# Kernel tuning notes

Measured on AMD Instinct MI355X. Metric: run time of the kernel, lower is better.

Reference implementation:

```python
import jax, jax.numpy as jnp
import numpy as np

N_NODES = 50000
N_EDGES = 800000
IN_DIM = 128
HID = 128
NUM_GRAPHS = 64


def setup_inputs() -> dict:
    key = jax.random.key(0)
    ks = jax.random.split(key, 10)
    x = jax.random.normal(ks[0], (N_NODES, IN_DIM), dtype=jnp.float32)
    edge_index = jax.random.randint(ks[1], (2, N_EDGES), 0, N_NODES, dtype=jnp.int64)
    batch = jnp.sort(jax.random.randint(ks[2], (N_NODES,), 0, NUM_GRAPHS, dtype=jnp.int64))
    s = 1.0 / np.sqrt(IN_DIM)
    W0 = jax.random.uniform(ks[3], (IN_DIM, HID), jnp.float32, -s, s)
    b0 = jnp.zeros((HID,), jnp.float32)
    s = 1.0 / np.sqrt(HID)
    W1 = jax.random.uniform(ks[4], (HID, HID), jnp.float32, -s, s)
    b1 = jnp.zeros((HID,), jnp.float32)
    W2 = jax.random.uniform(ks[5], (HID, HID), jnp.float32, -s, s)
    b2 = jnp.zeros((HID,), jnp.float32)
    return {"x": x, "edge_index": edge_index, "batch": batch,
            "W0": W0, "b0": b0, "W1": W1, "b1": b1, "W2": W2, "b2": b2}


def reference(x, edge_index, batch, W0, b0, W1, b1, W2, b2):
    N = x.shape[0]
    # GCNConv: add self loops, symmetric degree normalization
    loop = jnp.arange(N, dtype=edge_index.dtype)
    src = jnp.concatenate([edge_index[0], loop])  # [E+N]
    dst = jnp.concatenate([edge_index[1], loop])
    deg = jax.ops.segment_sum(jnp.ones_like(dst, dtype=x.dtype), dst, num_segments=N)
    dinv = jnp.where(deg > 0, jax.lax.rsqrt(deg), 0.0)
    norm = (dinv[src] * dinv[dst])[:, None]  # [E+N, 1]

    def gcn_layer(h, W, b):
        h = h @ W  # [N, hid]
        agg = jax.ops.segment_sum(h[src] * norm, dst, num_segments=N)
        return agg + b

    h = jax.nn.relu(gcn_layer(x, W0, b0))
    h = jax.nn.relu(gcn_layer(h, W1, b1))
    h = jax.nn.relu(gcn_layer(h, W2, b2))
    # dropout is identity at inference (training=False)

    # global_mean_pool by batch index
    sums = jax.ops.segment_sum(h, batch, num_segments=NUM_GRAPHS)
    counts = jax.ops.segment_sum(jnp.ones((N,), h.dtype), batch, num_segments=NUM_GRAPHS)
    return sums / jnp.maximum(counts, 1.0)[:, None]
```

## Files before the change

kernel.cpp:

```cpp
#include <hip/hip_runtime.h>
#include <hip/hip_bf16.h>

#define NNODES 50000
#define NEDGES 800000
#define HIDDIM 128
#define NGRAPH 64
#define BUCKET 64

typedef __attribute__((ext_vector_type(8))) short short8;
typedef __attribute__((ext_vector_type(4))) float floatx4;
typedef __attribute__((ext_vector_type(4))) unsigned short ushortx4;
typedef __attribute__((ext_vector_type(4))) unsigned int uintx4;

__device__ __forceinline__ float bfbits2f(unsigned short u) {
    return __uint_as_float(((unsigned int)u) << 16);
}
__device__ __forceinline__ unsigned short f2bfbits(float v) {
    __hip_bfloat16 h = __float2bfloat16(v);
    return __builtin_bit_cast(unsigned short, h);
}
__device__ __forceinline__ float bflo(unsigned int w) { return __uint_as_float(w << 16); }
__device__ __forceinline__ float bfhi(unsigned int w) { return __uint_as_float(w & 0xffff0000u); }

__global__ void k_detect(const unsigned int* __restrict__ xw,
                         const unsigned int* __restrict__ eiw,
                         int* __restrict__ flags) {
    __shared__ int sh_hit, sh_zero;
    int t = threadIdx.x;
    if (t == 0) { sh_hit = 0; sh_zero = 0; }
    __syncthreads();
    if (t < 128) {
        unsigned int w = xw[t * 97 + 5];
        int e = (int)((w >> 7) & 0xFF);
        if (e >= 110 && e <= 140) atomicAdd(&sh_hit, 1);
        if (eiw[1001 + 2 * t] == 0) atomicAdd(&sh_zero, 1);
    }
    __syncthreads();
    if (t == 0) {
        flags[0] = (sh_hit >= 64) ? 1 : 0;
        flags[1] = (sh_zero >= 120) ? 1 : 0;
    }
}

__global__ void k_init(const unsigned int* __restrict__ xw,
                       const unsigned int* __restrict__ eiw,
                       int* __restrict__ flags, int* __restrict__ cnt) {
    __shared__ int sh_hit, sh_zero;
    int t = threadIdx.x;
    int i = blockIdx.x * 256 + t;
    if (i < 50176) cnt[i] = 0;
    if (blockIdx.x != 0) return;
    if (t == 0) { sh_hit = 0; sh_zero = 0; }
    __syncthreads();
    if (t < 128) {
        unsigned int w = xw[t * 97 + 5];
        int e = (int)((w >> 7) & 0xFF);
        if (e >= 110 && e <= 140) atomicAdd(&sh_hit, 1);
        if (eiw[1001 + 2 * t] == 0) atomicAdd(&sh_zero, 1);
    }
    __syncthreads();
    if (t == 0) {
        flags[0] = (sh_hit >= 64) ? 1 : 0;
        flags[1] = (sh_zero >= 120) ? 1 : 0;
    }
}

__device__ __forceinline__ int ld_idx(const int* __restrict__ p, int j, int wide) {
    return wide ? p[2 * j] : p[j];
}

__global__ __launch_bounds__(256) void k_append(const int* __restrict__ ei,
                                                const int* __restrict__ bat,
                                                const int* __restrict__ flags,
                                                int* __restrict__ cnt,
                                                unsigned short* __restrict__ ecol,
                                                int* __restrict__ bounds) {
    if (blockIdx.x == gridDim.x - 1) {
        int g = threadIdx.x;
        if (g > NGRAPH) return;
        int wide = flags[1];
        int lo = 0, hi = NNODES;
        while (lo < hi) {
            int mid = (lo + hi) >> 1;
            if (ld_idx(bat, mid, wide) < g) lo = mid + 1; else hi = mid;
        }
        bounds[g] = lo;
        return;
    }
    int T = blockIdx.x * 256 + threadIdx.x;
    int e0 = T * 8;
    if (e0 >= NEDGES) return;
    int wide = flags[1];
    int s[8], d[8];
    if (wide) {
        const int4* __restrict__ sp = (const int4*)ei;
        const int4* __restrict__ dp = (const int4*)(ei + 2 * NEDGES);
#pragma unroll
        for (int q = 0; q < 4; ++q) {
            int4 sv = sp[T * 4 + q]; s[2 * q] = sv.x; s[2 * q + 1] = sv.z;
            int4 dv = dp[T * 4 + q]; d[2 * q] = dv.x; d[2 * q + 1] = dv.z;
        }
    } else {
        const int4* __restrict__ sp = (const int4*)ei;
        const int4* __restrict__ dp = (const int4*)(ei + NEDGES);
#pragma unroll
        for (int q = 0; q < 2; ++q) {
            int4 sv = sp[T * 2 + q];
            s[4 * q] = sv.x; s[4 * q + 1] = sv.y; s[4 * q + 2] = sv.z; s[4 * q + 3] = sv.w;
            int4 dv = dp[T * 2 + q];
            d[4 * q] = dv.x; d[4 * q + 1] = dv.y; d[4 * q + 2] = dv.z; d[4 * q + 3] = dv.w;
        }
    }
    int p[8];
#pragma unroll
    for (int q = 0; q < 8; ++q) p[q] = atomicAdd(&cnt[d[q]], 1);
#pragma unroll
    for (int q = 0; q < 8; ++q) {
        if (p[q] < BUCKET) {
            __builtin_nontemporal_store((unsigned short)s[q],
                                        &ecol[(size_t)d[q] * BUCKET + p[q]]);
        }
    }
}

__global__ __launch_bounds__(256) void k_gemm_mfma(const void* __restrict__ A,
                                                   const void* __restrict__ W,
                                                   const int* __restrict__ flags,
                                                   int a_mode,
                                                   const int* __restrict__ degcnt,
                                                   unsigned short* __restrict__ out,
                                                   int M) {
    __shared__ __align__(16) unsigned short Wl[16 * 128 * 8];
    __shared__ __align__(16) unsigned short Alds[64 * 17 * 8];
    const int tid = threadIdx.x;
    const int F = flags[0];
    const int abf = (a_mode == 2) ? 1 : (a_mode == 1 ? F : 0);
    const int row0 = blockIdx.x * 64;

    if (F) {
        const ushort4* __restrict__ Wg = (const ushort4*)W;
#pragma unroll
        for (int it = 0; it < 16; ++it) {
            int idx = it * 256 + tid;
            int k = idx >> 5, n = (idx & 31) * 4;
            ushort4 wv = Wg[idx];
            unsigned short* dst = &Wl[(((k >> 3) * 128) + n) * 8 + (k & 7)];
            dst[0] = wv.x; dst[8] = wv.y; dst[16] = wv.z; dst[24] = wv.w;
        }
    } else {
        const float4* __restrict__ Wg = (const float4*)W;
#pragma unroll
        for (int it = 0; it < 16; ++it) {
            int idx = it * 256 + tid;
            int k = idx >> 5, n = (idx & 31) * 4;
            float4 wv = Wg[idx];
            unsigned short* dst = &Wl[(((k >> 3) * 128) + n) * 8 + (k & 7)];
            dst[0] = f2bfbits(wv.x); dst[8]  = f2bfbits(wv.y);
            dst[16] = f2bfbits(wv.z); dst[24] = f2bfbits(wv.w);
        }
    }
    if (abf) {
#pragma unroll
        for (int it = 0; it < 4; ++it) {
            int idx = it * 256 + tid;
            int m = idx >> 4, kb = idx & 15;
            int gr = row0 + m;
            uint4 v = make_uint4(0, 0, 0, 0);
            if (gr < M) v = ((const uint4*)A)[(size_t)gr * 16 + kb];
            *reinterpret_cast<uint4*>(&Alds[(m * 17 + kb) * 8]) = v;
        }
    } else {
#pragma unroll
        for (int it = 0; it < 8; ++it) {
            int idx = it * 256 + tid;
            int m = idx >> 5, k4 = idx & 31;
            int k = k4 * 4;
            int gr = row0 + m;
            float4 v = make_float4(0, 0, 0, 0);
            if (gr < M) v = ((const float4*)A)[(size_t)gr * 32 + k4];
            ushort4 u;
            u.x = f2bfbits(v.x); u.y = f2bfbits(v.y);
            u.z = f2bfbits(v.z); u.w = f2bfbits(v.w);
            *reinterpret_cast<ushort4*>(&Alds[(m * 17 + (k >> 3)) * 8 + (k & 7)]) = u;
        }
    }
    __syncthreads();

    const int lane = tid & 63;
    const int wave = tid >> 6;
    const int q = lane >> 4;
    const int c = lane & 15;
    const int mrow = wave * 16 + c;
    floatx4 acc[8] = {};
#pragma unroll
    for (int k0 = 0; k0 < 4; ++k0) {
        int kb = k0 * 4 + q;
        short8 afrag = *reinterpret_cast<const short8*>(&Alds[(mrow * 17 + kb) * 8]);
#pragma unroll
        for (int t = 0; t < 8; ++t) {
            short8 bfrag = *reinterpret_cast<const short8*>(&Wl[(kb * 128 + t * 16 + c) * 8]);
            acc[t] = __builtin_amdgcn_mfma_f32_16x16x32_bf16(afrag, bfrag, acc[t], 0, 0, 0);
        }
    }
#pragma unroll
    for (int i = 0; i < 4; ++i) {
        int gr = row0 + wave * 16 + q * 4 + i;
        if (gr < M) {
            float s = degcnt ? rsqrtf((float)degcnt[gr] + 1.0f) : 1.0f;
#pragma unroll
            for (int t = 0; t < 8; ++t) {
                out[(size_t)gr * 128 + t * 16 + c] = f2bfbits(acc[t][i] * s);
            }
        }
    }
}

__global__ __launch_bounds__(256) void k_gather(const int* __restrict__ cnt,
                                                const unsigned short* __restrict__ ecol,
                                                const unsigned short* __restrict__ tmp16,
                                                const void* __restrict__ bias,
                                                const int* __restrict__ flags,
                                                unsigned short* __restrict__ outh16) {
    int t = blockIdx.x * 256 + threadIdx.x;
    int n = t >> 4;
    if (n >= NNODES) return;
    int j = t & 15;
    int degf = cnt[n];
    float dn = rsqrtf((float)degf + 1.0f);
    int deg = degf > BUCKET ? BUCKET : degf;
    const unsigned short* __restrict__ bk = &ecol[(size_t)n * BUCKET];
    const uint4* __restrict__ base = reinterpret_cast<const uint4*>(tmp16);
    float a[8];
    {
        uint4 u = base[(size_t)n * 16 + j];
        a[0] = bflo(u.x); a[1] = bfhi(u.x);
        a[2] = bflo(u.y); a[3] = bfhi(u.y);
        a[4] = bflo(u.z); a[5] = bfhi(u.z);
        a[6] = bflo(u.w); a[7] = bfhi(u.w);
    }
    int k = 0;
    for (; k + 3 < deg; k += 4) {
        ushortx4 sv = __builtin_nontemporal_load(
            reinterpret_cast<const ushortx4*>(&bk[k]));
        uint4 u0 = base[(size_t)sv[0] * 16 + j];
        uint4 u1 = base[(size_t)sv[1] * 16 + j];
        uint4 u2 = base[(size_t)sv[2] * 16 + j];
        uint4 u3 = base[(size_t)sv[3] * 16 + j];
        a[0] += (bflo(u0.x) + bflo(u1.x)) + (bflo(u2.x) + bflo(u3.x));
        a[1] += (bfhi(u0.x) + bfhi(u1.x)) + (bfhi(u2.x) + bfhi(u3.x));
        a[2] += (bflo(u0.y) + bflo(u1.y)) + (bflo(u2.y) + bflo(u3.y));
        a[3] += (bfhi(u0.y) + bfhi(u1.y)) + (bfhi(u2.y) + bfhi(u3.y));
        a[4] += (bflo(u0.z) + bflo(u1.z)) + (bflo(u2.z) + bflo(u3.z));
        a[5] += (bfhi(u0.z) + bfhi(u1.z)) + (bfhi(u2.z) + bfhi(u3.z));
        a[6] += (bflo(u0.w) + bflo(u1.w)) + (bflo(u2.w) + bflo(u3.w));
        a[7] += (bfhi(u0.w) + bfhi(u1.w)) + (bfhi(u2.w) + bfhi(u3.w));
    }
    for (; k < deg; ++k) {
        uint4 u0 = base[(size_t)bk[k] * 16 + j];
        a[0] += bflo(u0.x); a[1] += bfhi(u0.x);
        a[2] += bflo(u0.y); a[3] += bfhi(u0.y);
        a[4] += bflo(u0.z); a[5] += bfhi(u0.z);
        a[6] += bflo(u0.w); a[7] += bfhi(u0.w);
    }
    float b[8];
    if (flags[0]) {
        uint4 bb = ((const uint4*)bias)[j];
        b[0] = bflo(bb.x); b[1] = bfhi(bb.x);
        b[2] = bflo(bb.y); b[3] = bfhi(bb.y);
        b[4] = bflo(bb.z); b[5] = bfhi(bb.z);
        b[6] = bflo(bb.w); b[7] = bfhi(bb.w);
    } else {
        float4 f0 = ((const float4*)bias)[2 * j];
        float4 f1 = ((const float4*)bias)[2 * j + 1];
        b[0] = f0.x; b[1] = f0.y; b[2] = f0.z; b[3] = f0.w;
        b[4] = f1.x; b[5] = f1.y; b[6] = f1.z; b[7] = f1.w;
    }
    uintx4 ov;
#pragma unroll
    for (int i2 = 0; i2 < 4; ++i2) {
        float r0 = fmaxf(a[2 * i2]     * dn + b[2 * i2],     0.0f);
        float r1 = fmaxf(a[2 * i2 + 1] * dn + b[2 * i2 + 1], 0.0f);
        ov[i2] = (unsigned int)f2bfbits(r0) | ((unsigned int)f2bfbits(r1) << 16);
    }
    __builtin_nontemporal_store(ov,
        reinterpret_cast<uintx4*>(outh16 + (size_t)n * 128 + j * 8));
}

__global__ __launch_bounds__(256) void k_gemm(const void* __restrict__ A,
                                              const void* __restrict__ W,
                                              const int* __restrict__ flags,
                                              int a_uses_flag,
                                              float* __restrict__ out, int M) {
    __shared__ __align__(16) float Al[32 * 128];
    const int tid = threadIdx.x;
    const int F = flags[0];
    const int afmt = a_uses_flag ? F : 0;
    const int row0 = blockIdx.x * 32;
#pragma unroll
    for (int j = 0; j < 16; ++j) {
        int idx = j * 256 + tid;
        int r = idx >> 7, k = idx & 127;
        int gr = row0 + r;
        float v = 0.0f;
        if (gr < M) {
            size_t off = (size_t)gr * 128 + k;
            v = afmt ? bfbits2f(((const unsigned short*)A)[off])
                     : ((const float*)A)[off];
        }
        Al[idx] = v;
    }
    __syncthreads();
    const int tx = tid & 31, ty = tid >> 5;
    const int c0 = tx * 4;
    float acc[4][4] = {};
    if (F) {
        const ushort4* __restrict__ Wg = (const ushort4*)W;
#pragma unroll 4
        for (int k = 0; k < 128; ++k) {
            ushort4 wv = Wg[k * 32 + tx];
            float w0 = bfbits2f(wv.x), w1 = bfbits2f(wv.y);
            float w2 = bfbits2f(wv.z), w3 = bfbits2f(wv.w);
#pragma unroll
            for (int i = 0; i < 4; ++i) {
                float a = Al[(ty + i * 8) * 128 + k];
                acc[i][0] = fmaf(a, w0, acc[i][0]);
                acc[i][1] = fmaf(a, w1, acc[i][1]);
                acc[i][2] = fmaf(a, w2, acc[i][2]);
                acc[i][3] = fmaf(a, w3, acc[i][3]);
            }
        }
    } else {
        const float4* __restrict__ Wg = (const float4*)W;
#pragma unroll 4
        for (int k = 0; k < 128; ++k) {
            float4 wv = Wg[k * 32 + tx];
#pragma unroll
            for (int i = 0; i < 4; ++i) {
                float a = Al[(ty + i * 8) * 128 + k];
                acc[i][0] = fmaf(a, wv.x, acc[i][0]);
                acc[i][1] = fmaf(a, wv.y, acc[i][1]);
                acc[i][2] = fmaf(a, wv.z, acc[i][2]);
                acc[i][3] = fmaf(a, wv.w, acc[i][3]);
            }
        }
    }
#pragma unroll
    for (int i = 0; i < 4; ++i) {
        int gr = row0 + ty + i * 8;
        if (gr < M) {
            *reinterpret_cast<float4*>(&out[(size_t)gr * 128 + c0]) =
                make_float4(acc[i][0], acc[i][1], acc[i][2], acc[i][3]);
        }
    }
}
__global__ void k_deg_init(float* __restrict__ deg) {
    int i = blockIdx.x * 256 + threadIdx.x;
    if (i < NNODES) deg[i] = 1.0f;
}
__global__ void k_deg_edges(const int* __restrict__ ei, const int* __restrict__ flags,
                            float* __restrict__ deg) {
    int e = blockIdx.x * 256 + threadIdx.x;
    if (e < NEDGES) unsafeAtomicAdd(&deg[ld_idx(ei, NEDGES + e, flags[1])], 1.0f);
}
__global__ void k_rsqrt(float* __restrict__ deg) {
    int i = blockIdx.x * 256 + threadIdx.x;
    if (i < NNODES) deg[i] = 1.0f / sqrtf(deg[i]);
}
__global__ void k_selfloop(const float* __restrict__ tmp, const float* __restrict__ dinv,
                           float* __restrict__ agg) {
    int t = blockIdx.x * 256 + threadIdx.x;
    if (t >= NNODES * 32) return;
    int n = t >> 5, j = t & 31;
    float s = dinv[n]; s = s * s;
    float4 v = *reinterpret_cast<const float4*>(&tmp[(size_t)n * 128 + j * 4]);
    v.x *= s; v.y *= s; v.z *= s; v.w *= s;
    *reinterpret_cast<float4*>(&agg[(size_t)n * 128 + j * 4]) = v;
}
__global__ __launch_bounds__(256) void k_scatter(const int* __restrict__ ei,
                                                 const int* __restrict__ flags,
                                                 const float* __restrict__ dinv,
                                                 const float* __restrict__ tmp,
                                                 float* __restrict__ agg) {
    int t = blockIdx.x * 256 + threadIdx.x;
    int e = t >> 5;
    if (e >= NEDGES) return;
    int j = t & 31;
    int wide = flags[1];
    int s = ld_idx(ei, e, wide);
    int d = ld_idx(ei, NEDGES + e, wide);
    float w = dinv[s] * dinv[d];
    const float4 v = *reinterpret_cast<const float4*>(&tmp[(size_t)s * 128 + j * 4]);
    float* p = &agg[(size_t)d * 128 + j * 4];
    unsafeAtomicAdd(p + 0, v.x * w);
    unsafeAtomicAdd(p + 1, v.y * w);
    unsafeAtomicAdd(p + 2, v.z * w);
    unsafeAtomicAdd(p + 3, v.w * w);
}
__global__ void k_bias_relu(float* __restrict__ h, const void* __restrict__ b,
                            const int* __restrict__ flags) {
    int t = blockIdx.x * 256 + threadIdx.x;
    if (t >= NNODES * 32) return;
    int j = t & 31;
    float b0, b1, b2, b3;
    if (flags[0]) {
        const unsigned short* bb = (const unsigned short*)b;
        b0 = bfbits2f(bb[j * 4 + 0]); b1 = bfbits2f(bb[j * 4 + 1]);
        b2 = bfbits2f(bb[j * 4 + 2]); b3 = bfbits2f(bb[j * 4 + 3]);
    } else {
        const float* bb = (const float*)b;
        b0 = bb[j * 4 + 0]; b1 = bb[j * 4 + 1]; b2 = bb[j * 4 + 2]; b3 = bb[j * 4 + 3];
    }
    float4 v = *reinterpret_cast<float4*>(&h[(size_t)t * 4]);
    v.x = fmaxf(v.x + b0, 0.0f);
    v.y = fmaxf(v.y + b1, 0.0f);
    v.z = fmaxf(v.z + b2, 0.0f);
    v.w = fmaxf(v.w + b3, 0.0f);
    *reinterpret_cast<float4*>(&h[(size_t)t * 4]) = v;
}

__global__ void k_bounds(const int* __restrict__ batch, const int* __restrict__ flags,
                         int* __restrict__ bounds) {
    int g = threadIdx.x;
    if (g > NGRAPH) return;
    int wide = flags[1];
    int lo = 0, hi = NNODES;
    while (lo < hi) {
        int mid = (lo + hi) >> 1;
        if (ld_idx(batch, mid, wide) < g) lo = mid + 1; else hi = mid;
    }
    bounds[g] = lo;
}

__global__ __launch_bounds__(256) void k_pool_part(const unsigned short* __restrict__ h16,
                                                   const int* __restrict__ bounds,
                                                   float* __restrict__ part) {
    __shared__ float sh[256 * 4];
    int g = blockIdx.x >> 2, seg = blockIdx.x & 3;
    int t = threadIdx.x;
    int c4 = t & 31, sub = t >> 5;
    int beg = bounds[g], end = bounds[g + 1];
    const ushort4* __restrict__ base = (const ushort4*)h16;
    float ax = 0, ay = 0, az = 0, aw = 0;
    for (int r = beg + seg * 8 + sub; r < end; r += 32) {
        ushort4 u = base[(size_t)r * 32 + c4];
        ax += bfbits2f(u.x); ay += bfbits2f(u.y);
        az += bfbits2f(u.z); aw += bfbits2f(u.w);
    }
    sh[t * 4 + 0] = ax; sh[t * 4 + 1] = ay; sh[t * 4 + 2] = az; sh[t * 4 + 3] = aw;
    __syncthreads();
    if (t < 32) {
        float4 r = make_float4(0, 0, 0, 0);
#pragma unroll
        for (int s = 0; s < 8; ++s) {
            r.x += sh[(s * 32 + t) * 4 + 0];
            r.y += sh[(s * 32 + t) * 4 + 1];
            r.z += sh[(s * 32 + t) * 4 + 2];
            r.w += sh[(s * 32 + t) * 4 + 3];
        }
        *reinterpret_cast<float4*>(&part[((size_t)(g * 4 + seg)) * 128 + t * 4]) = r;
    }
}

__global__ void k_pool_final(const float* __restrict__ part, const int* __restrict__ bounds,
                             const int* __restrict__ flags, void* __restrict__ out) {
    int i = blockIdx.x * 256 + threadIdx.x;
    if (i >= NGRAPH * 128) return;
    int g = i >> 7, col = i & 127;
    float s = part[(g * 4 + 0) * 128 + col] + part[(g * 4 + 1) * 128 + col] +
              part[(g * 4 + 2) * 128 + col] + part[(g * 4 + 3) * 128 + col];
    float c = (float)(bounds[g + 1] - bounds[g]);
    float r = s / fmaxf(c, 1.0f);
    if (flags[0]) ((__hip_bfloat16*)out)[i] = __float2bfloat16(r);
    else          ((float*)out)[i] = r;
}

__global__ __launch_bounds__(1024) void k_pool2(const float* __restrict__ h,
                                                const int* __restrict__ bounds,
                                                const int* __restrict__ flags,
                                                void* __restrict__ out) {
    __shared__ float sh[1024];
    int g = blockIdx.x;
    int t = threadIdx.x;
    int beg = bounds[g], end = bounds[g + 1];
    int col = t & 127, seg = t >> 7;
    float acc = 0.0f;
    for (int r = beg + seg; r < end; r += 8)
        acc += h[(size_t)r * 128 + col];
    sh[t] = acc;
    __syncthreads();
    if (t < 128) {
        float total = 0.0f;
#pragma unroll
        for (int i = 0; i < 8; ++i) total += sh[t + 128 * i];
        float c = (float)(end - beg);
        float r = total / fmaxf(c, 1.0f);
        if (flags[0]) ((__hip_bfloat16*)out)[g * 128 + t] = __float2bfloat16(r);
        else          ((float*)out)[g * 128 + t] = r;
    }
}

extern "C" void kernel_launch(void* const* d_in, const int* in_sizes, int n_in,
                              void* d_out, int out_size, void* d_ws, size_t ws_size,
                              hipStream_t stream) {
    const void* x  = d_in[0];
    const int* ei  = (const int*)d_in[1];
    const int* bat = (const int*)d_in[2];
    const void* W0 = d_in[3];
    const void* b0 = d_in[4];
    const void* W1 = d_in[5];
    const void* b1 = d_in[6];
    const void* W2 = d_in[7];
    const void* b2 = d_in[8];

    float* ws = (float*)d_ws;
    size_t off = 0;
    int*   flags  = (int*)ws;           off += 16;
    float* dinv   = ws + off;           off += 50176;
    float* hA     = ws + off;           off += (size_t)NNODES * 128;
    float* hB     = ws + off;           off += (size_t)NNODES * 128;
    int*   bounds = (int*)(ws + off);   off += 80;
    int*   cnt    = (int*)(ws + off);   off += 50304;
    float* part   = ws + off;           off += NGRAPH * 4 * 128 + 64;
    const size_t needed = off * 4;
    unsigned short* hA16 = (unsigned short*)hA;
    unsigned short* hB16 = (unsigned short*)hB;
    unsigned short* ecol = (unsigned short*)(hA + (size_t)NNODES * 64);

    const int bN  = (NNODES + 255) / 256;
    const int bE  = (NEDGES + 255) / 256;
    const int bNF = (NNODES * 32) / 256;
    const int bEF = (NEDGES * 32) / 256;
    const int bA8 = (NEDGES / 8 + 255) / 256;
    const int bGT = (NNODES * 16) / 256;
    const int bG  = (NNODES + 31) / 32;
    const int bG2 = (NNODES + 63) / 64;
    dim3 blk(256);

    const bool use_csr = (ws_size >= needed);

    if (use_csr) {
        hipLaunchKernelGGL(k_init, dim3(bN), blk, 0, stream,
                           (const unsigned int*)x, (const unsigned int*)ei, flags, cnt);
        hipLaunchKernelGGL(k_append, dim3(bA8 + 1), blk, 0, stream,
                           ei, bat, flags, cnt, ecol, bounds);

        hipLaunchKernelGGL(k_gemm_mfma, dim3(bG2), blk, 0, stream, x,    W0, flags, 1, cnt, hA16, NNODES);
        hipLaunchKernelGGL(k_gather,    dim3(bGT), blk, 0, stream, cnt, ecol, hA16, b0, flags, hB16);
        hipLaunchKernelGGL(k_gemm_mfma, dim3(bG2), blk, 0, stream, hB16, W1, flags, 2, cnt, hA16, NNODES);
        hipLaunchKernelGGL(k_gather,    dim3(bGT), blk, 0, stream, cnt, ecol, hA16, b1, flags, hB16);
        hipLaunchKernelGGL(k_gemm_mfma, dim3(bG2), blk, 0, stream, hB16, W2, flags, 2, cnt, hA16, NNODES);
        hipLaunchKernelGGL(k_gather,    dim3(bGT), blk, 0, stream, cnt, ecol, hA16, b2, flags, hB16);

        hipLaunchKernelGGL(k_pool_part, dim3(NGRAPH * 4), blk, 0, stream, hB16, bounds, part);
        hipLaunchKernelGGL(k_pool_final, dim3(32), blk, 0, stream, part, bounds, flags, d_out);
    } else {
        hipLaunchKernelGGL(k_detect, dim3(1), blk, 0, stream,
                           (const unsigned int*)x, (const unsigned int*)ei, flags);
        hipLaunchKernelGGL(k_deg_init, dim3(bN), blk, 0, stream, dinv);
        hipLaunchKernelGGL(k_deg_edges, dim3(bE), blk, 0, stream, ei, flags, dinv);
        hipLaunchKernelGGL(k_rsqrt, dim3(bN), blk, 0, stream, dinv);

        hipLaunchKernelGGL(k_gemm, dim3(bG), blk, 0, stream, x, W0, flags, 1, hA, NNODES);
        hipLaunchKernelGGL(k_selfloop, dim3(bNF), blk, 0, stream, hA, dinv, hB);
        hipLaunchKernelGGL(k_scatter, dim3(bEF), blk, 0, stream, ei, flags, dinv, hA, hB);
        hipLaunchKernelGGL(k_bias_relu, dim3(bNF), blk, 0, stream, hB, b0, flags);

        hipLaunchKernelGGL(k_gemm, dim3(bG), blk, 0, stream, hB, W1, flags, 0, hA, NNODES);
        hipLaunchKernelGGL(k_selfloop, dim3(bNF), blk, 0, stream, hA, dinv, hB);
        hipLaunchKernelGGL(k_scatter, dim3(bEF), blk, 0, stream, ei, flags, dinv, hA, hB);
        hipLaunchKernelGGL(k_bias_relu, dim3(bNF), blk, 0, stream, hB, b1, flags);

        hipLaunchKernelGGL(k_gemm, dim3(bG), blk, 0, stream, hB, W2, flags, 0, hA, NNODES);
        hipLaunchKernelGGL(k_selfloop, dim3(bNF), blk, 0, stream, hA, dinv, hB);
        hipLaunchKernelGGL(k_scatter, dim3(bEF), blk, 0, stream, ei, flags, dinv, hA, hB);
        hipLaunchKernelGGL(k_bias_relu, dim3(bNF), blk, 0, stream, hB, b2, flags);

        hipLaunchKernelGGL(k_bounds, dim3(1), dim3(128), 0, stream, bat, flags, bounds);
        hipLaunchKernelGGL(k_pool2, dim3(NGRAPH), dim3(1024), 0, stream, hB, bounds, flags, d_out);
    }
}
```

Measured before the change: 331.7 us.

## Fuse neighbor gather with next layer's MFMA GEMM in one kernel

Adds a k_fused kernel in which each 64-row block gathers and normalizes neighbor features, applies bias and ReLU, and stages the bf16 rows in LDS. It then multiplies them by the next layer's weights with MFMA and writes the degree-scaled result. This replaces two gather+GEMM pairs and removes one full write and read of the intermediate hidden tensor per layer, plus two launches. The trade-off is less gather parallelism: 64 blocks of nodes per 256 threads with a serial loop over 4 groups, instead of one 16-thread group per node across the whole grid, which may hurt latency hiding on the irregular gathers.

```diff
diff --git a/kernel.cpp b/kernel.cpp
--- a/kernel.cpp
+++ b/kernel.cpp
@@ -207,6 +207,144 @@
         int gr = row0 + wave * 16 + q * 4 + i;
         if (gr < M) {
             float s = degcnt ? rsqrtf((float)degcnt[gr] + 1.0f) : 1.0f;
+#pragma unroll
+            for (int t = 0; t < 8; ++t) {
+                out[(size_t)gr * 128 + t * 16 + c] = f2bfbits(acc[t][i] * s);
+            }
+        }
+    }
+}
+
+__global__ __launch_bounds__(256) void k_fused(const int* __restrict__ cnt,
+                                               const unsigned short* __restrict__ ecol,
+                                               const unsigned short* __restrict__ tmp16,
+                                               const void* __restrict__ bias,
+                                               const void* __restrict__ W,
+                                               const int* __restrict__ flags,
+                                               unsigned short* __restrict__ out,
+                                               int M) {
+    __shared__ __align__(16) unsigned short Wl[16 * 128 * 8];
+    __shared__ __align__(16) unsigned short Alds[64 * 17 * 8];
+    const int tid = threadIdx.x;
+    const int F = flags[0];
+    const int row0 = blockIdx.x * 64;
+
+    if (F) {
+        const ushort4* __restrict__ Wg = (const ushort4*)W;
+#pragma unroll
+        for (int it = 0; it < 16; ++it) {
+            int idx = it * 256 + tid;
+            int k = idx >> 5, n = (idx & 31) * 4;
+            ushort4 wv = Wg[idx];
+            unsigned short* dst = &Wl[(((k >> 3) * 128) + n) * 8 + (k & 7)];
+            dst[0] = wv.x; dst[8] = wv.y; dst[16] = wv.z; dst[24] = wv.w;
+        }
+    } else {
+        const float4* __restrict__ Wg = (const float4*)W;
+#pragma unroll
+        for (int it = 0; it < 16; ++it) {
+            int idx = it * 256 + tid;
+            int k = idx >> 5, n = (idx & 31) * 4;
+            float4 wv = Wg[idx];
+            unsigned short* dst = &Wl[(((k >> 3) * 128) + n) * 8 + (k & 7)];
+            dst[0] = f2bfbits(wv.x); dst[8]  = f2bfbits(wv.y);
+            dst[16] = f2bfbits(wv.z); dst[24] = f2bfbits(wv.w);
+        }
+    }
+
+    {
+        const uint4* __restrict__ base = reinterpret_cast<const uint4*>(tmp16);
+        const int jl = tid & 15;
+        const int nsub = tid >> 4;
+        float b[8];
+        if (F) {
+            uint4 bb = ((const uint4*)bias)[jl];
+            b[0] = bflo(bb.x); b[1] = bfhi(bb.x);
+            b[2] = bflo(bb.y); b[3] = bfhi(bb.y);
+            b[4] = bflo(bb.z); b[5] = bfhi(bb.z);
+            b[6] = bflo(bb.w); b[7] = bfhi(bb.w);
+        } else {
+            float4 f0 = ((const float4*)bias)[2 * jl];
+            float4 f1 = ((const float4*)bias)[2 * jl + 1];
+            b[0] = f0.x; b[1] = f0.y; b[2] = f0.z; b[3] = f0.w;
+            b[4] = f1.x; b[5] = f1.y; b[6] = f1.z; b[7] = f1.w;
+        }
+#pragma unroll
+        for (int grp = 0; grp < 4; ++grp) {
+            int m = grp * 16 + nsub;
+            int n = row0 + m;
+            float a[8] = {0, 0, 0, 0, 0, 0, 0, 0};
+            float dn = 1.0f;
+            bool live = (n < M);
+            if (live) {
+                int degf = cnt[n];
+                dn = rsqrtf((float)degf + 1.0f);
+                int deg = degf > BUCKET ? BUCKET : degf;
+                const unsigned short* __restrict__ bk = &ecol[(size_t)n * BUCKET];
+                uint4 u = base[(size_t)n * 16 + jl];
+                a[0] = bflo(u.x); a[1] = bfhi(u.x);
+                a[2] = bflo(u.y); a[3] = bfhi(u.y);
+                a[4] = bflo(u.z); a[5] = bfhi(u.z);
+                a[6] = bflo(u.w); a[7] = bfhi(u.w);
+                int k = 0;
+                for (; k + 3 < deg; k += 4) {
+                    ushortx4 sv = __builtin_nontemporal_load(
+                        reinterpret_cast<const ushortx4*>(&bk[k]));
+                    uint4 u0 = base[(size_t)sv[0] * 16 + jl];
+                    uint4 u1 = base[(size_t)sv[1] * 16 + jl];
+                    uint4 u2 = base[(size_t)sv[2] * 16 + jl];
+                    uint4 u3 = base[(size_t)sv[3] * 16 + jl];
+                    a[0] += (bflo(u0.x) + bflo(u1.x)) + (bflo(u2.x) + bflo(u3.x));
+                    a[1] += (bfhi(u0.x) + bfhi(u1.x)) + (bfhi(u2.x) + bfhi(u3.x));
+                    a[2] += (bflo(u0.y) + bflo(u1.y)) + (bflo(u2.y) + bflo(u3.y));
+                    a[3] += (bfhi(u0.y) + bfhi(u1.y)) + (bfhi(u2.y) + bfhi(u3.y));
+                    a[4] += (bflo(u0.z) + bflo(u1.z)) + (bflo(u2.z) + bflo(u3.z));
+                    a[5] += (bfhi(u0.z) + bfhi(u1.z)) + (bfhi(u2.z) + bfhi(u3.z));
+                    a[6] += (bflo(u0.w) + bflo(u1.w)) + (bflo(u2.w) + bflo(u3.w));
+                    a[7] += (bfhi(u0.w) + bfhi(u1.w)) + (bfhi(u2.w) + bfhi(u3.w));
+                }
+                for (; k < deg; ++k) {
+                    uint4 u0 = base[(size_t)bk[k] * 16 + jl];
+                    a[0] += bflo(u0.x); a[1] += bfhi(u0.x);
+                    a[2] += bflo(u0.y); a[3] += bfhi(u0.y);
+                    a[4] += bflo(u0.z); a[5] += bfhi(u0.z);
+                    a[6] += bflo(u0.w); a[7] += bfhi(u0.w);
+                }
+            }
+            unsigned int ow[4];
+#pragma unroll
+            for (int i2 = 0; i2 < 4; ++i2) {
+                float r0 = live ? fmaxf(a[2 * i2]     * dn + b[2 * i2],     0.0f) : 0.0f;
+                float r1 = live ? fmaxf(a[2 * i2 + 1] * dn + b[2 * i2 + 1], 0.0f) : 0.0f;
+                ow[i2] = (unsigned int)f2bfbits(r0) | ((unsigned int)f2bfbits(r1) << 16);
+            }
+            *reinterpret_cast<uint4*>(&Alds[(m * 17 + jl) * 8]) =
+                make_uint4(ow[0], ow[1], ow[2], ow[3]);
+        }
+    }
+    __syncthreads();
+
+    const int lane = tid & 63;
+    const int wave = tid >> 6;
+    const int q = lane >> 4;
+    const int c = lane & 15;
+    const int mrow = wave * 16 + c;
+    floatx4 acc[8] = {};
+#pragma unroll
+    for (int k0 = 0; k0 < 4; ++k0) {
+        int kb = k0 * 4 + q;
+        short8 afrag = *reinterpret_cast<const short8*>(&Alds[(mrow * 17 + kb) * 8]);
+#pragma unroll
+        for (int t = 0; t < 8; ++t) {
+            short8 bfrag = *reinterpret_cast<const short8*>(&Wl[(kb * 128 + t * 16 + c) * 8]);
+            acc[t] = __builtin_amdgcn_mfma_f32_16x16x32_bf16(afrag, bfrag, acc[t], 0, 0, 0);
+        }
+    }
+#pragma unroll
+    for (int i = 0; i < 4; ++i) {
+        int gr = row0 + wave * 16 + q * 4 + i;
+        if (gr < M) {
+            float s = rsqrtf((float)cnt[gr] + 1.0f);
 #pragma unroll
             for (int t = 0; t < 8; ++t) {
                 out[(size_t)gr * 128 + t * 16 + c] = f2bfbits(acc[t][i] * s);
@@ -544,12 +682,10 @@
         hipLaunchKernelGGL(k_append, dim3(bA8 + 1), blk, 0, stream,
                            ei, bat, flags, cnt, ecol, bounds);
 
-        hipLaunchKernelGGL(k_gemm_mfma, dim3(bG2), blk, 0, stream, x,    W0, flags, 1, cnt, hA16, NNODES);
-        hipLaunchKernelGGL(k_gather,    dim3(bGT), blk, 0, stream, cnt, ecol, hA16, b0, flags, hB16);
-        hipLaunchKernelGGL(k_gemm_mfma, dim3(bG2), blk, 0, stream, hB16, W1, flags, 2, cnt, hA16, NNODES);
-        hipLaunchKernelGGL(k_gather,    dim3(bGT), blk, 0, stream, cnt, ecol, hA16, b1, flags, hB16);
-        hipLaunchKernelGGL(k_gemm_mfma, dim3(bG2), blk, 0, stream, hB16, W2, flags, 2, cnt, hA16, NNODES);
-        hipLaunchKernelGGL(k_gather,    dim3(bGT), blk, 0, stream, cnt, ecol, hA16, b2, flags, hB16);
+        hipLaunchKernelGGL(k_gemm_mfma, dim3(bG2), blk, 0, stream, x, W0, flags, 1, cnt, hA16, NNODES);
+        hipLaunchKernelGGL(k_fused, dim3(bG2), blk, 0, stream, cnt, ecol, hA16, b0, W1, flags, hB16, NNODES);
+        hipLaunchKernelGGL(k_fused, dim3(bG2), blk, 0, stream, cnt, ecol, hB16, b1, W2, flags, hA16, NNODES);
+        hipLaunchKernelGGL(k_gather, dim3(bGT), blk, 0, stream, cnt, ecol, hA16, b2, flags, hB16);
 
         hipLaunchKernelGGL(k_pool_part, dim3(NGRAPH * 4), blk, 0, stream, hB16, bounds, part);
         hipLaunchKernelGGL(k_pool_final, dim3(32), blk, 0, stream, part, bounds, flags, d_out);
```

After: 341.4 us. 1.03x slower.
